# Kernel tuning notes

Hardware: AMD Instinct MI355X
Metric: run time of the kernel (lower is better)

## Reference

```python
import jax, jax.numpy as jnp
import numpy as np

B, C1, C2, H, W = 8, 256, 256, 64, 64
C = 256            # int(c1*e)
G = C // 16        # 16 groups (dg)
Cg = C // G        # 16 channels per group
K = 9              # 3x3 kernel sample points
BN_EPS = 1e-5

# kernel grid offsets for 3x3, dilation 1 (pad=1 centers the grid)
KH = jnp.array([-1, -1, -1, 0, 0, 0, 1, 1, 1], jnp.float32)
KW = jnp.array([-1, 0, 1, -1, 0, 1, -1, 0, 1], jnp.float32)


def setup_inputs() -> dict:
    key = jax.random.key(0)
    ks = jax.random.split(key, 10)
    x = jax.random.normal(ks[0], (B, C1, H, W), jnp.float32)
    w_cv1 = jax.random.normal(ks[1], (C, C1), jnp.float32) / np.sqrt(C1)
    b_cv1 = jax.random.normal(ks[2], (C,), jnp.float32) * 0.1
    # offset/mask linear (DCNv4 inits to zero; small scale keeps sampling sane)
    w_off = jax.random.normal(ks[3], (G * 3 * K, C), jnp.float32) * 0.01
    b_off = jax.random.normal(ks[4], (G * 3 * K,), jnp.float32) * 0.01
    w_cv2 = jax.random.normal(ks[5], (C2, C), jnp.float32) / np.sqrt(C)
    bn_gamma = jax.random.uniform(ks[6], (C2,), jnp.float32, 0.5, 1.5)
    bn_beta = jax.random.normal(ks[7], (C2,), jnp.float32) * 0.1
    bn_mean = jax.random.normal(ks[8], (C2,), jnp.float32) * 0.1
    bn_var = jax.random.uniform(ks[9], (C2,), jnp.float32, 0.5, 1.5)
    return dict(x=x, w_cv1=w_cv1, b_cv1=b_cv1, w_off=w_off, b_off=b_off,
                w_cv2=w_cv2, bn_gamma=bn_gamma, bn_beta=bn_beta,
                bn_mean=bn_mean, bn_var=bn_var)


def _gather(vflat, hi, wi):
    # vflat: (B, H*W, G, Cg); hi/wi: (B,H,W,K,G) float corner indices
    ok = ((hi >= 0) & (hi < H) & (wi >= 0) & (wi < W)).astype(vflat.dtype)
    idx = (jnp.clip(hi, 0, H - 1) * W + jnp.clip(wi, 0, W - 1)).astype(jnp.int32)
    idx = idx.reshape(B, H * W * K, G)
    idxb = jnp.broadcast_to(idx[..., None], (B, H * W * K, G, Cg))
    g = jnp.take_along_axis(vflat, idxb, axis=1)  # (B, HWK, G, Cg)
    return g.reshape(B, H, W, K, G, Cg), ok


def _dcnv4(v, off, mask):
    # v: (B,H,W,G,Cg); off: (B,H,W,G,K,2) (dh,dw); mask: (B,H,W,G,K)
    ii = jnp.arange(H, dtype=jnp.float32)
    jj = jnp.arange(W, dtype=jnp.float32)
    ph = ii[None, :, None, None, None] + KH[None, None, None, None, :] + off[..., 0]
    pw = jj[None, None, :, None, None] + KW[None, None, None, None, :] + off[..., 1]
    ph = ph.transpose(0, 1, 2, 4, 3)  # (B,H,W,K,G)
    pw = pw.transpose(0, 1, 2, 4, 3)
    h0 = jnp.floor(ph); w0 = jnp.floor(pw)
    ah = ph - h0; aw = pw - w0
    vflat = v.reshape(B, H * W, G, Cg)
    g00, ok00 = _gather(vflat, h0, w0)
    g01, ok01 = _gather(vflat, h0, w0 + 1)
    g10, ok10 = _gather(vflat, h0 + 1, w0)
    g11, ok11 = _gather(vflat, h0 + 1, w0 + 1)
    w00 = ((1 - ah) * (1 - aw) * ok00)[..., None]
    w01 = ((1 - ah) * aw * ok01)[..., None]
    w10 = (ah * (1 - aw) * ok10)[..., None]
    w11 = (ah * aw * ok11)[..., None]
    sample = w00 * g00 + w01 * g01 + w10 * g10 + w11 * g11  # (B,H,W,K,G,Cg)
    out = jnp.einsum('bhwkgc,bhwgk->bhwgc', sample, mask)
    return out.reshape(B, H, W, C).transpose(0, 3, 1, 2)  # NCHW


def reference(x, w_cv1, b_cv1, w_off, b_off, w_cv2, bn_gamma, bn_beta, bn_mean, bn_var):
    # cv1: 1x1 conv
    h1 = jnp.einsum('bchw,oc->bohw', x, w_cv1) + b_cv1[None, :, None, None]
    # offset/mask 1x1 projection, per-group layout [2K offsets, K masks]
    om = jnp.einsum('bchw,oc->bhwo', h1, w_off) + b_off
    om = om.reshape(B, H, W, G, 3 * K)
    off = om[..., :2 * K].reshape(B, H, W, G, K, 2)
    mask = om[..., 2 * K:]  # DCNv4: no softmax, used directly
    v = h1.transpose(0, 2, 3, 1).reshape(B, H, W, G, Cg)
    y = _dcnv4(v, off, mask)
    # cv2: 1x1 conv (no bias)
    y = jnp.einsum('bchw,oc->bohw', y, w_cv2)
    # BatchNorm (eval mode)
    scale = (bn_gamma / jnp.sqrt(bn_var + BN_EPS))[None, :, None, None]
    y = (y - bn_mean[None, :, None, None]) * scale + bn_beta[None, :, None, None]
    # SiLU
    return y * jax.nn.sigmoid(y)
```

## Files before the change

### kernel.cpp

```cpp
#include <hip/hip_runtime.h>

#define HW 4096
#define CCH 256
#define MOFF 432
#define PTOT 32768
#define PDIM 68
#define PIMG (PDIM*PDIM)

typedef unsigned short u16;
typedef __attribute__((ext_vector_type(8))) short short8;
typedef __attribute__((ext_vector_type(8))) unsigned short u16x8;
typedef __attribute__((ext_vector_type(4))) unsigned short u16x4;
typedef __attribute__((ext_vector_type(4))) float f32x4;

__device__ __forceinline__ u16 f2b(float f){
  unsigned int u = __float_as_uint(f);
  unsigned int rounding = 0x7FFFu + ((u >> 16) & 1u);
  return (u16)((u + rounding) >> 16);
}
__device__ __forceinline__ float b2f(u16 s){
  return __uint_as_float(((unsigned int)s) << 16);
}

__global__ __launch_bounds__(256) void k_cvtw(const float* __restrict__ w1,
    const float* __restrict__ w2,
    const float* __restrict__ gamma, const float* __restrict__ beta,
    const float* __restrict__ mean, const float* __restrict__ var,
    u16* __restrict__ wb_big, u16* __restrict__ wb2,
    float* __restrict__ bnA, float* __restrict__ bnB, u16* __restrict__ h1p){
  int r = blockIdx.x, t = threadIdx.x;
  if (r < 256) wb_big[r*256 + t] = f2b(w1[r*256 + t]);
  else if (r < 336){ wb_big[(688 + (r - 256)) * 256 / 1 + t] = 0; }
  else if (r < 592){ int o = r - 336; wb2[o*256 + t] = f2b(w2[o*256 + t]); }
  else if (r == 592){
    if (t < 256){
      float sc = gamma[t] * rsqrtf(var[t] + 1e-5f);
      bnA[t] = sc;
      bnB[t] = beta[t] - mean[t] * sc;
    }
  } else {
    int n = (r - 593) * 128 + (t >> 1);
    int seg = t & 1;
    int plane = n / 528, m = n % 528;
    int row, col;
    if (m < 136){ row = m / 68; col = m % 68; }
    else if (m < 272){ int mm = m - 136; row = 66 + mm / 68; col = mm % 68; }
    else { int mm = m - 272; row = 2 + (mm >> 2); int c4 = mm & 3; col = (c4 & 1) + 66 * (c4 >> 1); }
    u16x8 z = {};
    *reinterpret_cast<u16x8*>(&h1p[((size_t)plane * PIMG + row * PDIM + col) * 16 + seg * 8]) = z;
  }
}

__global__ __launch_bounds__(256) void k_wcomb(const float* __restrict__ w1,
    const float* __restrict__ woff, const float* __restrict__ b1,
    const float* __restrict__ boff,
    u16* __restrict__ wb_big, float* __restrict__ bcomb){
  __shared__ float wr_[256];
  __shared__ float pb[256];
  const int j = blockIdx.x, t = threadIdx.x;
  wr_[t] = woff[j * 256 + t];
  __syncthreads();
  float s = 0.f;
  #pragma unroll 8
  for (int m = 0; m < 256; ++m) s += wr_[m] * w1[m * 256 + t];
  wb_big[(256 + j) * 256 + t] = f2b(s);
  pb[t] = wr_[t] * b1[t];
  __syncthreads();
  if (t == 0){
    float bs = boff[j];
    for (int m = 0; m < 256; ++m) bs += pb[m];
    bcomb[j] = bs;
  }
}

__global__ __launch_bounds__(256) void k_xt(const float* __restrict__ x,
    u16* __restrict__ xT){
  __shared__ float tile[64][65];
  const int pb = blockIdx.x * 64, cb = blockIdx.y * 64, b = blockIdx.z;
  const int t = threadIdx.x;
  const float* src = x + ((size_t)(b * CCH + cb)) * HW + pb;
  #pragma unroll
  for (int pass = 0; pass < 4; ++pass){
    int c_l = pass * 16 + (t >> 4);
    int pq = (t & 15) * 4;
    float4 v = *reinterpret_cast<const float4*>(&src[(size_t)c_l * HW + pq]);
    tile[pq + 0][c_l] = v.x; tile[pq + 1][c_l] = v.y;
    tile[pq + 2][c_l] = v.z; tile[pq + 3][c_l] = v.w;
  }
  __syncthreads();
  #pragma unroll
  for (int pass = 0; pass < 4; ++pass){
    int p_l = pass * 16 + (t >> 4);
    int cq = (t & 15) * 4;
    u16x4 o4;
    #pragma unroll
    for (int j = 0; j < 4; ++j) o4[j] = f2b(tile[p_l][cq + j]);
    *reinterpret_cast<u16x4*>(&xT[((size_t)b * HW + pb + p_l) * CCH + cb + cq]) = o4;
  }
}

__global__ __launch_bounds__(256) void k_gemm_big(const u16* __restrict__ A,
    const u16* __restrict__ Bw, const float* __restrict__ b1,
    const float* __restrict__ bcomb, u16* __restrict__ h1p,
    u16* __restrict__ om){
  __shared__ __align__(16) u16 smem[128 * 136];
  const int bid = blockIdx.x;
  const int xcd = bid & 7, s = bid >> 3;
  const int row_local = s / 6, cblk = s % 6;
  const int tm = (row_local * 8 + xcd) * 128;
  const int tn = cblk * 128;

  const int t = threadIdx.x;
  const int lane = t & 63;
  const int wid = t >> 6;
  const int wr = wid >> 1, wc = wid & 1;
  constexpr int BOFF = 128 * 40;

  f32x4 acc[4][4] = {};

  for (int kc = 0; kc < 256; kc += 32){
    #pragma unroll
    for (int i = 0; i < 2; ++i){
      int v = t + i * 256;
      int row = v >> 2, cq = v & 3;
      *reinterpret_cast<u16x8*>(&smem[row * 40 + cq * 8]) =
        *reinterpret_cast<const u16x8*>(&A[(size_t)(tm + row) * 256 + kc + cq * 8]);
    }
    #pragma unroll
    for (int i = 0; i < 2; ++i){
      int v = t + i * 256;
      int row = v >> 2, cq = v & 3;
      *reinterpret_cast<u16x8*>(&smem[BOFF + row * 40 + cq * 8]) =
        *reinterpret_cast<const u16x8*>(&Bw[(size_t)(tn + row) * 256 + kc + cq * 8]);
    }
    __syncthreads();
    short8 af[4], bf[4];
    #pragma unroll
    for (int m = 0; m < 4; ++m)
      af[m] = *reinterpret_cast<const short8*>(
        &smem[(wr * 64 + m * 16 + (lane & 15)) * 40 + (lane >> 4) * 8]);
    #pragma unroll
    for (int n = 0; n < 4; ++n)
      bf[n] = *reinterpret_cast<const short8*>(
        &smem[BOFF + (wc * 64 + n * 16 + (lane & 15)) * 40 + (lane >> 4) * 8]);
    #pragma unroll
    for (int m = 0; m < 4; ++m)
      #pragma unroll
      for (int n = 0; n < 4; ++n)
        acc[m][n] = __builtin_amdgcn_mfma_f32_16x16x32_bf16(af[m], bf[n], acc[m][n], 0, 0, 0);
    __syncthreads();
  }

  constexpr int CP = 136;
  u16* C_l = smem;
  #pragma unroll
  for (int n = 0; n < 4; ++n){
    int col = wc * 64 + n * 16 + (lane & 15);
    int o = tn + col;
    float bi = (o < 256) ? b1[o] : ((o - 256 < MOFF) ? bcomb[o - 256] : 0.f);
    #pragma unroll
    for (int m = 0; m < 4; ++m){
      int r0 = wr * 64 + m * 16 + ((lane >> 4) << 2);
      #pragma unroll
      for (int j = 0; j < 4; ++j)
        C_l[(r0 + j) * CP + col] = f2b(acc[m][n][j] + bi);
    }
  }
  __syncthreads();
  #pragma unroll
  for (int pass = 0; pass < 8; ++pass){
    int row = pass * 16 + (t >> 4);
    int sg = t & 15;
    int oc = tn + sg * 8;
    int p = tm + row;
    if (tn < 256){
      int bb = p >> 12, ii = (p >> 6) & 63, jj = p & 63;
      size_t dst = ((size_t)(bb * 16 + (oc >> 4)) * PIMG + (ii + 2) * PDIM + jj + 2) * 16 + (oc & 15);
      *reinterpret_cast<u16x8*>(&h1p[dst]) =
        *reinterpret_cast<const u16x8*>(&C_l[row * CP + sg * 8]);
    } else {
      int occ = oc - 256;
      if (occ + 8 <= MOFF)
        *reinterpret_cast<u16x8*>(&om[(size_t)p * MOFF + occ]) =
          *reinterpret_cast<const u16x8*>(&C_l[row * CP + sg * 8]);
    }
  }
}

__global__ __launch_bounds__(256) void k_gemm2(const u16* __restrict__ A,
    const u16* __restrict__ Bw, const float* __restrict__ bnA,
    const float* __restrict__ bnB, float* __restrict__ out){
  __shared__ __align__(16) u16 smem[(128 + 128) * 40];
  const int t = threadIdx.x;
  const int tm = blockIdx.x * 128;
  const int tn = blockIdx.y * 128;
  const int lane = t & 63;
  const int wid = t >> 6;
  const int wr = wid >> 1, wc = wid & 1;
  constexpr int BOFF = 128 * 40;

  f32x4 acc[4][4] = {};

  for (int kc = 0; kc < 256; kc += 32){
    #pragma unroll
    for (int i = 0; i < 2; ++i){
      int v = t + i * 256;
      int row = v >> 2, cq = v & 3;
      *reinterpret_cast<u16x8*>(&smem[row * 40 + cq * 8]) =
        *reinterpret_cast<const u16x8*>(&A[(size_t)(tm + row) * 256 + kc + cq * 8]);
    }
    #pragma unroll
    for (int i = 0; i < 2; ++i){
      int v = t + i * 256;
      int row = v >> 2, cq = v & 3;
      *reinterpret_cast<u16x8*>(&smem[BOFF + row * 40 + cq * 8]) =
        *reinterpret_cast<const u16x8*>(&Bw[(size_t)(tn + row) * 256 + kc + cq * 8]);
    }
    __syncthreads();
    short8 af[4], bf[4];
    #pragma unroll
    for (int m = 0; m < 4; ++m)
      af[m] = *reinterpret_cast<const short8*>(
        &smem[(wr * 64 + m * 16 + (lane & 15)) * 40 + (lane >> 4) * 8]);
    #pragma unroll
    for (int n = 0; n < 4; ++n)
      bf[n] = *reinterpret_cast<const short8*>(
        &smem[BOFF + (wc * 64 + n * 16 + (lane & 15)) * 40 + (lane >> 4) * 8]);
    #pragma unroll
    for (int m = 0; m < 4; ++m)
      #pragma unroll
      for (int n = 0; n < 4; ++n)
        acc[m][n] = __builtin_amdgcn_mfma_f32_16x16x32_bf16(af[m], bf[n], acc[m][n], 0, 0, 0);
    __syncthreads();
  }

  const int bimg = tm >> 12;
  const int ploc = tm & 4095;
  #pragma unroll
  for (int n = 0; n < 4; ++n){
    int o = tn + wc * 64 + n * 16 + (lane & 15);
    float sA = bnA[o], sB = bnB[o];
    #pragma unroll
    for (int m = 0; m < 4; ++m){
      int prow = wr * 64 + m * 16 + ((lane >> 4) << 2);
      f32x4 st;
      #pragma unroll
      for (int j = 0; j < 4; ++j){
        float y = acc[m][n][j] * sA + sB;
        st[j] = y / (1.f + expf(-y));
      }
      *reinterpret_cast<f32x4*>(&out[((size_t)(bimg * 256 + o)) * HW + ploc + prow]) = st;
    }
  }
}

__global__ __launch_bounds__(256) void k_sample(const u16* __restrict__ h1p,
    const u16* __restrict__ om, u16* __restrict__ ydcn){
  __shared__ float oms[4 * MOFF];
  const int t = threadIdx.x;
  const int pblk = blockIdx.x * 4;
  if (t < 216){
    u16x8 v = *reinterpret_cast<const u16x8*>(&om[(size_t)pblk * MOFF + t * 8]);
    float4 lo, hi;
    lo.x = b2f(v[0]); lo.y = b2f(v[1]); lo.z = b2f(v[2]); lo.w = b2f(v[3]);
    hi.x = b2f(v[4]); hi.y = b2f(v[5]); hi.z = b2f(v[6]); hi.w = b2f(v[7]);
    *reinterpret_cast<float4*>(&oms[t * 8]) = lo;
    *reinterpret_cast<float4*>(&oms[t * 8 + 4]) = hi;
  }
  __syncthreads();

  const int px = t >> 6;
  const int g = (t >> 2) & 15;
  const int q = t & 3;
  const int p = pblk + px;
  const int b = p >> 12, hw = p & 4095;
  const int ic = hw >> 6, jc = hw & 63;
  const u16* plane = h1p + (size_t)(b * 16 + g) * PIMG * 16;
  const float* ob = &oms[px * MOFF + g * 27];
  const float fi = (float)ic, fj = (float)jc;
  const bool wsel = (q >= 2);

  float acc[8] = {};
  #pragma unroll
  for (int k = 0; k < 9; ++k){
    float oh = ob[2 * k], ow = ob[2 * k + 1], m = ob[18 + k];
    float ph = fi + (float)(k / 3 - 1) + oh;
    float pw = fj + (float)(k % 3 - 1) + ow;
    float h0f = floorf(ph), w0f = floorf(pw);
    float ah = ph - h0f, aw = pw - w0f;
    int h0 = (int)h0f, w0 = (int)w0f;
    int hc = min(max(h0, -2), 64) + 2;
    int wc = min(max(w0, -2), 64) + 2;
    const u16* cbase = plane + ((hc * PDIM + wc) << 4) + (q << 3);
    u16x8 tv = *reinterpret_cast<const u16x8*>(cbase);
    u16x8 bv = *reinterpret_cast<const u16x8*>(cbase + PDIM * 16);
    float mh1 = m * ah, mh0 = m - mh1;
    float awq = wsel ? aw : (1.f - aw);
    float ct = mh0 * awq, cb = mh1 * awq;
    #pragma unroll
    for (int j = 0; j < 8; ++j)
      acc[j] += ct * b2f(tv[j]) + cb * b2f(bv[j]);
  }
  #pragma unroll
  for (int j = 0; j < 8; ++j)
    acc[j] += __shfl_xor(acc[j], 2, 64);
  if (q < 2){
    u16x8 o8;
    #pragma unroll
    for (int j = 0; j < 8; ++j) o8[j] = f2b(acc[j]);
    *reinterpret_cast<u16x8*>(&ydcn[(size_t)p * 256 + g * 16 + q * 8]) = o8;
  }
}

extern "C" void kernel_launch(void* const* d_in, const int* in_sizes, int n_in,
                              void* d_out, int out_size, void* d_ws, size_t ws_size,
                              hipStream_t stream) {
  const float* x     = (const float*)d_in[0];
  const float* w1    = (const float*)d_in[1];
  const float* b1    = (const float*)d_in[2];
  const float* woff  = (const float*)d_in[3];
  const float* boff  = (const float*)d_in[4];
  const float* w2    = (const float*)d_in[5];
  const float* gamma = (const float*)d_in[6];
  const float* beta  = (const float*)d_in[7];
  const float* mean  = (const float*)d_in[8];
  const float* var   = (const float*)d_in[9];
  float* out = (float*)d_out;
  (void)in_sizes; (void)n_in; (void)out_size; (void)ws_size;

  u16* h1p    = (u16*)d_ws;
  u16* om     = h1p + (size_t)128 * PIMG * 16;
  u16* xT     = om + (size_t)PTOT * MOFF;
  u16* ydcn   = xT;
  u16* wb_big = xT + (size_t)PTOT * CCH;
  u16* wb2    = wb_big + 768 * 256;
  float* bnA  = (float*)(wb2 + 256 * 256);
  float* bnB  = bnA + 256;
  float* bcomb = bnB + 256;

  dim3 blk(256);
  k_cvtw<<<dim3(1121), blk, 0, stream>>>(w1, w2, gamma, beta, mean, var,
                                         wb_big, wb2, bnA, bnB, h1p);
  k_wcomb<<<dim3(432), blk, 0, stream>>>(w1, woff, b1, boff, wb_big, bcomb);
  k_xt<<<dim3(64, 4, 8), blk, 0, stream>>>(x, xT);
  k_gemm_big<<<dim3(1536), blk, 0, stream>>>(xT, wb_big, b1, bcomb, h1p, om);
  k_sample<<<dim3(PTOT / 4), blk, 0, stream>>>(h1p, om, ydcn);
  k_gemm2<<<dim3(PTOT / 128, 2), blk, 0, stream>>>(ydcn, wb2, bnA, bnB, out);
}
```

Measured before the change: 104.4 us.

## Fuse x transpose/convert into first GEMM and merge weight-combine into prep kernel

Removes the separate k_xt transpose kernel. The first GEMM now reads fp32 NCHW x directly, transposes it through a padded LDS tile and converts it to bf16 inside its K loop. The weight-combine kernel is merged into the weight-conversion kernel as extra blocks, cutting two launches and the xT round trip through global memory. In exchange, each of the six column blocks per row tile re-reads and re-converts the same x data, and each K step gains an extra LDS pass and barrier.

```diff
diff --git a/kernel.cpp b/kernel.cpp
--- a/kernel.cpp
+++ b/kernel.cpp
@@ -23,14 +23,17 @@
 }
 
 __global__ __launch_bounds__(256) void k_cvtw(const float* __restrict__ w1,
-    const float* __restrict__ w2,
+    const float* __restrict__ w2, const float* __restrict__ woff,
+    const float* __restrict__ b1, const float* __restrict__ boff,
     const float* __restrict__ gamma, const float* __restrict__ beta,
     const float* __restrict__ mean, const float* __restrict__ var,
     u16* __restrict__ wb_big, u16* __restrict__ wb2,
-    float* __restrict__ bnA, float* __restrict__ bnB, u16* __restrict__ h1p){
+    float* __restrict__ bnA, float* __restrict__ bnB,
+    float* __restrict__ bcomb, u16* __restrict__ h1p){
+  __shared__ float sbuf[512];
   int r = blockIdx.x, t = threadIdx.x;
   if (r < 256) wb_big[r*256 + t] = f2b(w1[r*256 + t]);
-  else if (r < 336){ wb_big[(688 + (r - 256)) * 256 / 1 + t] = 0; }
+  else if (r < 336){ wb_big[(688 + (r - 256)) * 256 + t] = 0; }
   else if (r < 592){ int o = r - 336; wb2[o*256 + t] = f2b(w2[o*256 + t]); }
   else if (r == 592){
     if (t < 256){
@@ -38,7 +41,7 @@
       bnA[t] = sc;
       bnB[t] = beta[t] - mean[t] * sc;
     }
-  } else {
+  } else if (r < 1121){
     int n = (r - 593) * 128 + (t >> 1);
     int seg = t & 1;
     int plane = n / 528, m = n % 528;
@@ -48,62 +51,36 @@
     else { int mm = m - 272; row = 2 + (mm >> 2); int c4 = mm & 3; col = (c4 & 1) + 66 * (c4 >> 1); }
     u16x8 z = {};
     *reinterpret_cast<u16x8*>(&h1p[((size_t)plane * PIMG + row * PDIM + col) * 16 + seg * 8]) = z;
-  }
-}
-
-__global__ __launch_bounds__(256) void k_wcomb(const float* __restrict__ w1,
-    const float* __restrict__ woff, const float* __restrict__ b1,
-    const float* __restrict__ boff,
-    u16* __restrict__ wb_big, float* __restrict__ bcomb){
-  __shared__ float wr_[256];
-  __shared__ float pb[256];
-  const int j = blockIdx.x, t = threadIdx.x;
-  wr_[t] = woff[j * 256 + t];
-  __syncthreads();
-  float s = 0.f;
-  #pragma unroll 8
-  for (int m = 0; m < 256; ++m) s += wr_[m] * w1[m * 256 + t];
-  wb_big[(256 + j) * 256 + t] = f2b(s);
-  pb[t] = wr_[t] * b1[t];
-  __syncthreads();
-  if (t == 0){
-    float bs = boff[j];
-    for (int m = 0; m < 256; ++m) bs += pb[m];
-    bcomb[j] = bs;
-  }
-}
-
-__global__ __launch_bounds__(256) void k_xt(const float* __restrict__ x,
-    u16* __restrict__ xT){
-  __shared__ float tile[64][65];
-  const int pb = blockIdx.x * 64, cb = blockIdx.y * 64, b = blockIdx.z;
-  const int t = threadIdx.x;
-  const float* src = x + ((size_t)(b * CCH + cb)) * HW + pb;
-  #pragma unroll
-  for (int pass = 0; pass < 4; ++pass){
-    int c_l = pass * 16 + (t >> 4);
-    int pq = (t & 15) * 4;
-    float4 v = *reinterpret_cast<const float4*>(&src[(size_t)c_l * HW + pq]);
-    tile[pq + 0][c_l] = v.x; tile[pq + 1][c_l] = v.y;
-    tile[pq + 2][c_l] = v.z; tile[pq + 3][c_l] = v.w;
-  }
-  __syncthreads();
-  #pragma unroll
-  for (int pass = 0; pass < 4; ++pass){
-    int p_l = pass * 16 + (t >> 4);
-    int cq = (t & 15) * 4;
-    u16x4 o4;
-    #pragma unroll
-    for (int j = 0; j < 4; ++j) o4[j] = f2b(tile[p_l][cq + j]);
-    *reinterpret_cast<u16x4*>(&xT[((size_t)b * HW + pb + p_l) * CCH + cb + cq]) = o4;
-  }
-}
-
-__global__ __launch_bounds__(256) void k_gemm_big(const u16* __restrict__ A,
+  } else {
+    float* wr_ = sbuf;
+    float* pb  = sbuf + 256;
+    const int j = r - 1121;
+    wr_[t] = woff[j * 256 + t];
+    __syncthreads();
+    float s = 0.f;
+    #pragma unroll 8
+    for (int m = 0; m < 256; ++m) s += wr_[m] * w1[m * 256 + t];
+    wb_big[(256 + j) * 256 + t] = f2b(s);
+    pb[t] = wr_[t] * b1[t];
+    __syncthreads();
+    if (t == 0){
+      float bs = boff[j];
+      for (int m = 0; m < 256; ++m) bs += pb[m];
+      bcomb[j] = bs;
+    }
+  }
+}
+
+__global__ __launch_bounds__(256) void k_gemm_big(const float* __restrict__ x,
     const u16* __restrict__ Bw, const float* __restrict__ b1,
     const float* __restrict__ bcomb, u16* __restrict__ h1p,
     u16* __restrict__ om){
-  __shared__ __align__(16) u16 smem[128 * 136];
+  __shared__ __align__(16) unsigned char smraw[37376];
+  u16*   As = (u16*)smraw;
+  u16*   Bs = (u16*)(smraw + 10240);
+  float* ft = (float*)(smraw + 20480);
+  u16*  C_l = (u16*)smraw;
+
   const int bid = blockIdx.x;
   const int xcd = bid & 7, s = bid >> 3;
   const int row_local = s / 6, cblk = s % 6;
@@ -114,35 +91,50 @@
   const int lane = t & 63;
   const int wid = t >> 6;
   const int wr = wid >> 1, wc = wid & 1;
-  constexpr int BOFF = 128 * 40;
+  const int bb = tm >> 12, ploc = tm & 4095;
 
   f32x4 acc[4][4] = {};
 
   for (int kc = 0; kc < 256; kc += 32){
+    #pragma unroll
+    for (int i = 0; i < 4; ++i){
+      int idx = t + i * 256;
+      int c_l = idx >> 5, p4 = (idx & 31) * 4;
+      float4 v = *reinterpret_cast<const float4*>(
+        &x[((size_t)(bb * 256 + kc + c_l)) * HW + ploc + p4]);
+      ft[(p4 + 0) * 33 + c_l] = v.x;
+      ft[(p4 + 1) * 33 + c_l] = v.y;
+      ft[(p4 + 2) * 33 + c_l] = v.z;
+      ft[(p4 + 3) * 33 + c_l] = v.w;
+    }
     #pragma unroll
     for (int i = 0; i < 2; ++i){
       int v = t + i * 256;
       int row = v >> 2, cq = v & 3;
-      *reinterpret_cast<u16x8*>(&smem[row * 40 + cq * 8]) =
-        *reinterpret_cast<const u16x8*>(&A[(size_t)(tm + row) * 256 + kc + cq * 8]);
-    }
+      *reinterpret_cast<u16x8*>(&Bs[row * 40 + cq * 8]) =
+        *reinterpret_cast<const u16x8*>(&Bw[(size_t)(tn + row) * 256 + kc + cq * 8]);
+    }
+    __syncthreads();
     #pragma unroll
     for (int i = 0; i < 2; ++i){
-      int v = t + i * 256;
-      int row = v >> 2, cq = v & 3;
-      *reinterpret_cast<u16x8*>(&smem[BOFF + row * 40 + cq * 8]) =
-        *reinterpret_cast<const u16x8*>(&Bw[(size_t)(tn + row) * 256 + kc + cq * 8]);
+      int idx = t + i * 256;
+      int p = idx >> 2, cq = (idx & 3) * 8;
+      const float* fr = &ft[p * 33 + cq];
+      u16x8 o;
+      #pragma unroll
+      for (int j = 0; j < 8; ++j) o[j] = f2b(fr[j]);
+      *reinterpret_cast<u16x8*>(&As[p * 40 + cq]) = o;
     }
     __syncthreads();
     short8 af[4], bf[4];
     #pragma unroll
     for (int m = 0; m < 4; ++m)
       af[m] = *reinterpret_cast<const short8*>(
-        &smem[(wr * 64 + m * 16 + (lane & 15)) * 40 + (lane >> 4) * 8]);
+        &As[(wr * 64 + m * 16 + (lane & 15)) * 40 + (lane >> 4) * 8]);
     #pragma unroll
     for (int n = 0; n < 4; ++n)
       bf[n] = *reinterpret_cast<const short8*>(
-        &smem[BOFF + (wc * 64 + n * 16 + (lane & 15)) * 40 + (lane >> 4) * 8]);
+        &Bs[(wc * 64 + n * 16 + (lane & 15)) * 40 + (lane >> 4) * 8]);
     #pragma unroll
     for (int m = 0; m < 4; ++m)
       #pragma unroll
@@ -152,7 +144,6 @@
   }
 
   constexpr int CP = 136;
-  u16* C_l = smem;
   #pragma unroll
   for (int n = 0; n < 4; ++n){
     int col = wc * 64 + n * 16 + (lane & 15);
@@ -174,8 +165,8 @@
     int oc = tn + sg * 8;
     int p = tm + row;
     if (tn < 256){
-      int bb = p >> 12, ii = (p >> 6) & 63, jj = p & 63;
-      size_t dst = ((size_t)(bb * 16 + (oc >> 4)) * PIMG + (ii + 2) * PDIM + jj + 2) * 16 + (oc & 15);
+      int bb2 = p >> 12, ii = (p >> 6) & 63, jj = p & 63;
+      size_t dst = ((size_t)(bb2 * 16 + (oc >> 4)) * PIMG + (ii + 2) * PDIM + jj + 2) * 16 + (oc & 15);
       *reinterpret_cast<u16x8*>(&h1p[dst]) =
         *reinterpret_cast<const u16x8*>(&C_l[row * CP + sg * 8]);
     } else {
@@ -330,20 +321,18 @@
 
   u16* h1p    = (u16*)d_ws;
   u16* om     = h1p + (size_t)128 * PIMG * 16;
-  u16* xT     = om + (size_t)PTOT * MOFF;
-  u16* ydcn   = xT;
-  u16* wb_big = xT + (size_t)PTOT * CCH;
+  u16* ydcn   = om + (size_t)PTOT * MOFF;
+  u16* wb_big = ydcn + (size_t)PTOT * CCH;
   u16* wb2    = wb_big + 768 * 256;
   float* bnA  = (float*)(wb2 + 256 * 256);
   float* bnB  = bnA + 256;
   float* bcomb = bnB + 256;
 
   dim3 blk(256);
-  k_cvtw<<<dim3(1121), blk, 0, stream>>>(w1, w2, gamma, beta, mean, var,
-                                         wb_big, wb2, bnA, bnB, h1p);
-  k_wcomb<<<dim3(432), blk, 0, stream>>>(w1, woff, b1, boff, wb_big, bcomb);
-  k_xt<<<dim3(64, 4, 8), blk, 0, stream>>>(x, xT);
-  k_gemm_big<<<dim3(1536), blk, 0, stream>>>(xT, wb_big, b1, bcomb, h1p, om);
+  k_cvtw<<<dim3(1553), blk, 0, stream>>>(w1, w2, woff, b1, boff,
+                                         gamma, beta, mean, var,
+                                         wb_big, wb2, bnA, bnB, bcomb, h1p);
+  k_gemm_big<<<dim3(1536), blk, 0, stream>>>(x, wb_big, b1, bcomb, h1p, om);
   k_sample<<<dim3(PTOT / 4), blk, 0, stream>>>(h1p, om, ydcn);
   k_gemm2<<<dim3(PTOT / 128, 2), blk, 0, stream>>>(ydcn, wb2, bnA, bnB, out);
 }
```

Result: no change. 106.2 us (+1.8%).

## Merge prep kernels into one launch and enlarge first GEMM tile

Applied to the files above, without the earlier changes.

Folds the weight conversion, weight-combination and input transpose kernels into a single prep launch, removing two launch boundaries. The first GEMM moves from 128x128 tiles with K-step 32 to 256x128 tiles with K-step 64, adds launch bounds for two blocks per CU, and doubles per-warp accumulators to improve data reuse. ydcn gets its own workspace region instead of aliasing xT. The larger tile raises register and LDS pressure and halves the grid, which may reduce occupancy.

```diff
diff --git a/kernel.cpp b/kernel.cpp
--- a/kernel.cpp
+++ b/kernel.cpp
@@ -22,24 +22,50 @@
   return __uint_as_float(((unsigned int)s) << 16);
 }
 
-__global__ __launch_bounds__(256) void k_cvtw(const float* __restrict__ w1,
-    const float* __restrict__ w2,
+__global__ __launch_bounds__(256) void k_prep(const float* __restrict__ x,
+    const float* __restrict__ w1, const float* __restrict__ w2,
+    const float* __restrict__ woff, const float* __restrict__ b1,
+    const float* __restrict__ boff,
     const float* __restrict__ gamma, const float* __restrict__ beta,
     const float* __restrict__ mean, const float* __restrict__ var,
-    u16* __restrict__ wb_big, u16* __restrict__ wb2,
-    float* __restrict__ bnA, float* __restrict__ bnB, u16* __restrict__ h1p){
-  int r = blockIdx.x, t = threadIdx.x;
-  if (r < 256) wb_big[r*256 + t] = f2b(w1[r*256 + t]);
-  else if (r < 336){ wb_big[(688 + (r - 256)) * 256 / 1 + t] = 0; }
-  else if (r < 592){ int o = r - 336; wb2[o*256 + t] = f2b(w2[o*256 + t]); }
-  else if (r == 592){
+    u16* __restrict__ xT, u16* __restrict__ wb_big, u16* __restrict__ wb2,
+    float* __restrict__ bnA, float* __restrict__ bnB,
+    float* __restrict__ bcomb, u16* __restrict__ h1p){
+  __shared__ float tile[64][65];
+  const int r = blockIdx.x, t = threadIdx.x;
+  if (r < 2048){
+    const int pb = (r & 63) * 64, cb = ((r >> 6) & 3) * 64, b = r >> 8;
+    const float* src = x + ((size_t)(b * CCH + cb)) * HW + pb;
+    #pragma unroll
+    for (int pass = 0; pass < 4; ++pass){
+      int c_l = pass * 16 + (t >> 4);
+      int pq = (t & 15) * 4;
+      float4 v = *reinterpret_cast<const float4*>(&src[(size_t)c_l * HW + pq]);
+      tile[pq + 0][c_l] = v.x; tile[pq + 1][c_l] = v.y;
+      tile[pq + 2][c_l] = v.z; tile[pq + 3][c_l] = v.w;
+    }
+    __syncthreads();
+    #pragma unroll
+    for (int pass = 0; pass < 4; ++pass){
+      int p_l = pass * 16 + (t >> 4);
+      int cq = (t & 15) * 4;
+      u16x4 o4;
+      #pragma unroll
+      for (int j = 0; j < 4; ++j) o4[j] = f2b(tile[p_l][cq + j]);
+      *reinterpret_cast<u16x4*>(&xT[((size_t)b * HW + pb + p_l) * CCH + cb + cq]) = o4;
+    }
+  }
+  else if (r < 2304){ int o = r - 2048; wb_big[o*256 + t] = f2b(w1[o*256 + t]); }
+  else if (r < 2384){ wb_big[(688 + (r - 2304)) * 256 + t] = 0; }
+  else if (r < 2640){ int o = r - 2384; wb2[o*256 + t] = f2b(w2[o*256 + t]); }
+  else if (r == 2640){
     if (t < 256){
       float sc = gamma[t] * rsqrtf(var[t] + 1e-5f);
       bnA[t] = sc;
       bnB[t] = beta[t] - mean[t] * sc;
     }
-  } else {
-    int n = (r - 593) * 128 + (t >> 1);
+  } else if (r < 3169){
+    int n = (r - 2641) * 128 + (t >> 1);
     int seg = t & 1;
     int plane = n / 528, m = n % 528;
     int row, col;
@@ -48,106 +74,80 @@
     else { int mm = m - 272; row = 2 + (mm >> 2); int c4 = mm & 3; col = (c4 & 1) + 66 * (c4 >> 1); }
     u16x8 z = {};
     *reinterpret_cast<u16x8*>(&h1p[((size_t)plane * PIMG + row * PDIM + col) * 16 + seg * 8]) = z;
-  }
-}
-
-__global__ __launch_bounds__(256) void k_wcomb(const float* __restrict__ w1,
-    const float* __restrict__ woff, const float* __restrict__ b1,
-    const float* __restrict__ boff,
-    u16* __restrict__ wb_big, float* __restrict__ bcomb){
-  __shared__ float wr_[256];
-  __shared__ float pb[256];
-  const int j = blockIdx.x, t = threadIdx.x;
-  wr_[t] = woff[j * 256 + t];
-  __syncthreads();
-  float s = 0.f;
-  #pragma unroll 8
-  for (int m = 0; m < 256; ++m) s += wr_[m] * w1[m * 256 + t];
-  wb_big[(256 + j) * 256 + t] = f2b(s);
-  pb[t] = wr_[t] * b1[t];
-  __syncthreads();
-  if (t == 0){
-    float bs = boff[j];
-    for (int m = 0; m < 256; ++m) bs += pb[m];
-    bcomb[j] = bs;
-  }
-}
-
-__global__ __launch_bounds__(256) void k_xt(const float* __restrict__ x,
-    u16* __restrict__ xT){
-  __shared__ float tile[64][65];
-  const int pb = blockIdx.x * 64, cb = blockIdx.y * 64, b = blockIdx.z;
-  const int t = threadIdx.x;
-  const float* src = x + ((size_t)(b * CCH + cb)) * HW + pb;
-  #pragma unroll
-  for (int pass = 0; pass < 4; ++pass){
-    int c_l = pass * 16 + (t >> 4);
-    int pq = (t & 15) * 4;
-    float4 v = *reinterpret_cast<const float4*>(&src[(size_t)c_l * HW + pq]);
-    tile[pq + 0][c_l] = v.x; tile[pq + 1][c_l] = v.y;
-    tile[pq + 2][c_l] = v.z; tile[pq + 3][c_l] = v.w;
-  }
-  __syncthreads();
-  #pragma unroll
-  for (int pass = 0; pass < 4; ++pass){
-    int p_l = pass * 16 + (t >> 4);
-    int cq = (t & 15) * 4;
-    u16x4 o4;
-    #pragma unroll
-    for (int j = 0; j < 4; ++j) o4[j] = f2b(tile[p_l][cq + j]);
-    *reinterpret_cast<u16x4*>(&xT[((size_t)b * HW + pb + p_l) * CCH + cb + cq]) = o4;
-  }
-}
-
-__global__ __launch_bounds__(256) void k_gemm_big(const u16* __restrict__ A,
+  } else {
+    float* wr_ = &tile[0][0];
+    float* pb  = wr_ + 256;
+    const int j = r - 3169;
+    wr_[t] = woff[j * 256 + t];
+    __syncthreads();
+    float s = 0.f;
+    #pragma unroll 8
+    for (int m = 0; m < 256; ++m) s += wr_[m] * w1[m * 256 + t];
+    wb_big[(256 + j) * 256 + t] = f2b(s);
+    pb[t] = wr_[t] * b1[t];
+    __syncthreads();
+    if (t == 0){
+      float bs = boff[j];
+      for (int m = 0; m < 256; ++m) bs += pb[m];
+      bcomb[j] = bs;
+    }
+  }
+}
+
+__global__ __launch_bounds__(256, 2) void k_gemm_big(const u16* __restrict__ A,
     const u16* __restrict__ Bw, const float* __restrict__ b1,
     const float* __restrict__ bcomb, u16* __restrict__ h1p,
     u16* __restrict__ om){
-  __shared__ __align__(16) u16 smem[128 * 136];
+  __shared__ __align__(16) u16 smem[34816];
+  u16* As = smem;
+  u16* Bs = smem + 256 * 72;
+
   const int bid = blockIdx.x;
   const int xcd = bid & 7, s = bid >> 3;
   const int row_local = s / 6, cblk = s % 6;
-  const int tm = (row_local * 8 + xcd) * 128;
+  const int tm = (row_local * 8 + xcd) * 256;
   const int tn = cblk * 128;
 
   const int t = threadIdx.x;
   const int lane = t & 63;
   const int wid = t >> 6;
   const int wr = wid >> 1, wc = wid & 1;
-  constexpr int BOFF = 128 * 40;
-
-  f32x4 acc[4][4] = {};
-
-  for (int kc = 0; kc < 256; kc += 32){
-    #pragma unroll
-    for (int i = 0; i < 2; ++i){
-      int v = t + i * 256;
-      int row = v >> 2, cq = v & 3;
-      *reinterpret_cast<u16x8*>(&smem[row * 40 + cq * 8]) =
+
+  f32x4 acc[8][4] = {};
+
+  for (int kc = 0; kc < 256; kc += 64){
+    #pragma unroll
+    for (int i = 0; i < 8; ++i){
+      int idx = t + i * 256;
+      int row = idx >> 3, cq = idx & 7;
+      *reinterpret_cast<u16x8*>(&As[row * 72 + cq * 8]) =
         *reinterpret_cast<const u16x8*>(&A[(size_t)(tm + row) * 256 + kc + cq * 8]);
     }
     #pragma unroll
-    for (int i = 0; i < 2; ++i){
-      int v = t + i * 256;
-      int row = v >> 2, cq = v & 3;
-      *reinterpret_cast<u16x8*>(&smem[BOFF + row * 40 + cq * 8]) =
+    for (int i = 0; i < 4; ++i){
+      int idx = t + i * 256;
+      int row = idx >> 3, cq = idx & 7;
+      *reinterpret_cast<u16x8*>(&Bs[row * 72 + cq * 8]) =
         *reinterpret_cast<const u16x8*>(&Bw[(size_t)(tn + row) * 256 + kc + cq * 8]);
     }
     __syncthreads();
-    short8 af[4], bf[4];
-    #pragma unroll
-    for (int m = 0; m < 4; ++m)
-      af[m] = *reinterpret_cast<const short8*>(
-        &smem[(wr * 64 + m * 16 + (lane & 15)) * 40 + (lane >> 4) * 8]);
-    #pragma unroll
-    for (int n = 0; n < 4; ++n)
-      bf[n] = *reinterpret_cast<const short8*>(
-        &smem[BOFF + (wc * 64 + n * 16 + (lane & 15)) * 40 + (lane >> 4) * 8]);
-    #pragma unroll
-    for (int m = 0; m < 4; ++m)
+    #pragma unroll
+    for (int kk = 0; kk < 2; ++kk){
+      short8 af[8], bf[4];
+      #pragma unroll
+      for (int m = 0; m < 8; ++m)
+        af[m] = *reinterpret_cast<const short8*>(
+          &As[(wr * 128 + m * 16 + (lane & 15)) * 72 + kk * 32 + (lane >> 4) * 8]);
       #pragma unroll
       for (int n = 0; n < 4; ++n)
-        acc[m][n] = __builtin_amdgcn_mfma_f32_16x16x32_bf16(af[m], bf[n], acc[m][n], 0, 0, 0);
+        bf[n] = *reinterpret_cast<const short8*>(
+          &Bs[(wc * 64 + n * 16 + (lane & 15)) * 72 + kk * 32 + (lane >> 4) * 8]);
+      #pragma unroll
+      for (int m = 0; m < 8; ++m)
+        #pragma unroll
+        for (int n = 0; n < 4; ++n)
+          acc[m][n] = __builtin_amdgcn_mfma_f32_16x16x32_bf16(af[m], bf[n], acc[m][n], 0, 0, 0);
+    }
     __syncthreads();
   }
 
@@ -159,8 +159,8 @@
     int o = tn + col;
     float bi = (o < 256) ? b1[o] : ((o - 256 < MOFF) ? bcomb[o - 256] : 0.f);
     #pragma unroll
-    for (int m = 0; m < 4; ++m){
-      int r0 = wr * 64 + m * 16 + ((lane >> 4) << 2);
+    for (int m = 0; m < 8; ++m){
+      int r0 = wr * 128 + m * 16 + ((lane >> 4) << 2);
       #pragma unroll
       for (int j = 0; j < 4; ++j)
         C_l[(r0 + j) * CP + col] = f2b(acc[m][n][j] + bi);
@@ -168,7 +168,7 @@
   }
   __syncthreads();
   #pragma unroll
-  for (int pass = 0; pass < 8; ++pass){
+  for (int pass = 0; pass < 16; ++pass){
     int row = pass * 16 + (t >> 4);
     int sg = t & 15;
     int oc = tn + sg * 8;
@@ -331,19 +331,18 @@
   u16* h1p    = (u16*)d_ws;
   u16* om     = h1p + (size_t)128 * PIMG * 16;
   u16* xT     = om + (size_t)PTOT * MOFF;
-  u16* ydcn   = xT;
-  u16* wb_big = xT + (size_t)PTOT * CCH;
+  u16* ydcn   = xT + (size_t)PTOT * CCH;
+  u16* wb_big = ydcn + (size_t)PTOT * CCH;
   u16* wb2    = wb_big + 768 * 256;
   float* bnA  = (float*)(wb2 + 256 * 256);
   float* bnB  = bnA + 256;
   float* bcomb = bnB + 256;
 
   dim3 blk(256);
-  k_cvtw<<<dim3(1121), blk, 0, stream>>>(w1, w2, gamma, beta, mean, var,
-                                         wb_big, wb2, bnA, bnB, h1p);
-  k_wcomb<<<dim3(432), blk, 0, stream>>>(w1, woff, b1, boff, wb_big, bcomb);
-  k_xt<<<dim3(64, 4, 8), blk, 0, stream>>>(x, xT);
-  k_gemm_big<<<dim3(1536), blk, 0, stream>>>(xT, wb_big, b1, bcomb, h1p, om);
+  k_prep<<<dim3(3601), blk, 0, stream>>>(x, w1, w2, woff, b1, boff,
+                                         gamma, beta, mean, var,
+                                         xT, wb_big, wb2, bnA, bnB, bcomb, h1p);
+  k_gemm_big<<<dim3(768), blk, 0, stream>>>(xT, wb_big, b1, bcomb, h1p, om);
   k_sample<<<dim3(PTOT / 4), blk, 0, stream>>>(h1p, om, ydcn);
   k_gemm2<<<dim3(PTOT / 128, 2), blk, 0, stream>>>(ydcn, wb2, bnA, bnB, out);
 }
```

New measurement: 103.1 us. No clear change (-1.2%).
